# Kernel optimization log

Measured on AMD Instinct MI355X. Metric: run time of the kernel, lower is better.

The kernel has to match this reference:

```python
import jax, jax.numpy as jnp
import numpy as np

N = 100000
E = 1600000
D_IN = 128
D_OUT = 128


def setup_inputs() -> dict:
    key = jax.random.key(0)
    ks = jax.random.split(key, 6)
    seq = jax.random.normal(ks[0], (N, D_IN), dtype=jnp.float32)
    edge_src = jax.random.randint(ks[1], (E,), 0, N, dtype=jnp.int32)
    edge_dst = jax.random.randint(ks[2], (E,), 0, N, dtype=jnp.int32)
    adj_vals = jax.random.uniform(ks[3], (E,), dtype=jnp.float32)
    # xavier_uniform for [out, in] -> stored as [in, out] for x @ W
    lim = float(np.sqrt(6.0 / (D_IN + D_OUT)))
    w_fc = jax.random.uniform(ks[4], (D_IN, D_OUT), jnp.float32, -lim, lim)
    w_proj = jax.random.uniform(ks[5], (D_IN, D_OUT), jnp.float32, -lim, lim)
    b_proj = jnp.zeros((D_OUT,), jnp.float32)
    bias = jnp.zeros((D_OUT,), jnp.float32)
    return {"seq": seq, "edge_src": edge_src, "edge_dst": edge_dst,
            "adj_vals": adj_vals, "w_fc": w_fc, "w_proj": w_proj,
            "b_proj": b_proj, "bias": bias}


def reference(seq, edge_src, edge_dst, adj_vals, w_fc, w_proj, b_proj, bias):
    # h = fc(seq)  (no bias)
    h = seq @ w_fc                                  # [N, D_OUT]
    # spmm(adj, h): out[i] = sum_{e: dst=i} vals[e] * h[src[e]]
    msgs = adj_vals[:, None] * h[edge_src]          # [E, D_OUT]
    agg = jax.ops.segment_sum(msgs, edge_dst, num_segments=N)
    # bias add + residual proj(seq) add + tanh
    out = jnp.tanh(agg + bias + seq @ w_proj + b_proj)
    return out
```

## Files before the change

kernel.cpp:

```cpp
#include <hip/hip_runtime.h>
#include <math.h>


typedef __attribute__((ext_vector_type(8))) short short8;
typedef __attribute__((ext_vector_type(4))) float float4v;
typedef __attribute__((ext_vector_type(2))) _Float16 half2v;

#define PG 256
#define NBMAX 4096

static __device__ __forceinline__ short f2bf(float x) {
    unsigned u = __float_as_uint(x);
    unsigned r = (u + 0x7fffu + ((u >> 16) & 1u)) >> 16;
    return (short)r;
}
static __device__ __forceinline__ float bf2f(short h) {
    return __uint_as_float(((unsigned)(unsigned short)h) << 16);
}

__global__ __launch_bounds__(256)
void wconv_kernel(const float* __restrict__ wa, const float* __restrict__ wb,
                  short* __restrict__ whia, short* __restrict__ wloa,
                  short* __restrict__ whib, short* __restrict__ wlob) {
    const int bb = blockIdx.x;
    const float* w  = (bb < 16) ? wa   : wb;
    short* whi      = (bb < 16) ? whia : whib;
    short* wlo      = (bb < 16) ? wloa : wlob;
    const int i = (bb & 15) * 256 + threadIdx.x;
    const float4 v = ((const float4*)w)[i];
    const int k = i >> 5;
    const int c4 = (i & 31) * 4;
    float xs[4] = {v.x, v.y, v.z, v.w};
    #pragma unroll
    for (int j = 0; j < 4; j++) {
        const short hi = f2bf(xs[j]);
        const short lo = f2bf(xs[j] - bf2f(hi));
        whi[(c4 + j) * 128 + k] = hi;
        wlo[(c4 + j) * 128 + k] = lo;
    }
}

#define KP 136

__global__ __launch_bounds__(256, 2)
void mm_mfma_kernel(const float* __restrict__ seq, const short* __restrict__ whi,
                    const short* __restrict__ wlo,
                    const float* __restrict__ b0p, const float* __restrict__ b1p,
                    float* __restrict__ out, _Float16* __restrict__ out16,
                    int N, int add_bias) {
    __shared__ short wt_hi[128 * KP];
    __shared__ short wt_lo[128 * KP];

    const int tid = threadIdx.x;
    for (int i = tid; i < 2048; i += 256) {
        const int row = i >> 4;
        const int k8  = (i & 15) * 8;
        *(float4*)&wt_hi[row * KP + k8] = ((const float4*)whi)[i];
        *(float4*)&wt_lo[row * KP + k8] = ((const float4*)wlo)[i];
    }
    __syncthreads();

    const int wave = tid >> 6;
    const int lane = tid & 63;
    const int q = lane >> 4;
    const int c = lane & 15;
    const int R = blockIdx.x * 64 + wave * 16;
    const int rowL = (R + c < N) ? (R + c) : (N - 1);

    float4v acc[8];
    #pragma unroll
    for (int ct = 0; ct < 8; ct++) acc[ct] = (float4v){0.f, 0.f, 0.f, 0.f};

    #pragma unroll
    for (int t = 0; t < 4; t++) {
        const int kk = t * 32 + q * 8;
        const float4 a0 = *(const float4*)&seq[(size_t)rowL * 128 + kk];
        const float4 a1 = *(const float4*)&seq[(size_t)rowL * 128 + kk + 4];
        float xs[8] = {a0.x, a0.y, a0.z, a0.w, a1.x, a1.y, a1.z, a1.w};
        union { short s[8]; short8 v; } ahi, alo;
        #pragma unroll
        for (int j = 0; j < 8; j++) {
            const short hi = f2bf(xs[j]);
            ahi.s[j] = hi;
            alo.s[j] = f2bf(xs[j] - bf2f(hi));
        }
        #pragma unroll
        for (int ct = 0; ct < 8; ct++) {
            const int n = ct * 16 + c;
            const short8 bhi = *(const short8*)&wt_hi[n * KP + kk];
            const short8 blo = *(const short8*)&wt_lo[n * KP + kk];
            acc[ct] = __builtin_amdgcn_mfma_f32_16x16x32_bf16(ahi.v, bhi, acc[ct], 0, 0, 0);
            acc[ct] = __builtin_amdgcn_mfma_f32_16x16x32_bf16(ahi.v, blo, acc[ct], 0, 0, 0);
            acc[ct] = __builtin_amdgcn_mfma_f32_16x16x32_bf16(alo.v, bhi, acc[ct], 0, 0, 0);
        }
    }

    if (out16) {
        #pragma unroll
        for (int ct = 0; ct < 8; ct++) {
            const int col = ct * 16 + c;
            float badd = 0.f;
            if (add_bias) badd = b0p[col] + b1p[col];
            #pragma unroll
            for (int r = 0; r < 4; r++) {
                const int row = R + q * 4 + r;
                if (row < N) out16[(size_t)row * 128 + col] = (_Float16)(acc[ct][r] + badd);
            }
        }
    } else {
        #pragma unroll
        for (int ct = 0; ct < 8; ct++) {
            const int col = ct * 16 + c;
            float badd = 0.f;
            if (add_bias) badd = b0p[col] + b1p[col];
            #pragma unroll
            for (int r = 0; r < 4; r++) {
                const int row = R + q * 4 + r;
                if (row < N) out[(size_t)row * 128 + col] = acc[ct][r] + badd;
            }
        }
    }
}


__global__ __launch_bounds__(256)
void phist_kernel(const int* __restrict__ edst, int* __restrict__ hcnt,
                  int E, int S, int NB) {
    __shared__ int cnt[NBMAX];
    const int g = blockIdx.x;
    const int tid = threadIdx.x;
    for (int b = tid; b < NB; b += 256) cnt[b] = 0;
    __syncthreads();
    const int lo = g * S;
    const int hi = (lo + S < E) ? (lo + S) : E;
    for (int i = lo + tid; i < hi; i += 256)
        atomicAdd(&cnt[edst[i] >> 5], 1);
    __syncthreads();
    for (int b = tid; b < NB; b += 256) hcnt[b * PG + g] = cnt[b];
}

__global__ __launch_bounds__(256)
void pscan1_kernel(const int* __restrict__ in, int* __restrict__ out,
                   int* __restrict__ bsum, int L) {
    __shared__ int s[256];
    const int t = threadIdx.x;
    const int base = blockIdx.x * 4096 + t * 16;
    int v[16];
    int mysum = 0;
    #pragma unroll
    for (int j = 0; j < 16; j++) {
        v[j] = (base + j < L) ? in[base + j] : 0;
        mysum += v[j];
    }
    s[t] = mysum;
    __syncthreads();
    for (int o = 1; o < 256; o <<= 1) {
        int add = (t >= o) ? s[t - o] : 0;
        __syncthreads();
        s[t] += add;
        __syncthreads();
    }
    int run = s[t] - mysum;
    #pragma unroll
    for (int j = 0; j < 16; j++) {
        if (base + j < L) out[base + j] = run;
        run += v[j];
    }
    if (t == 255) bsum[blockIdx.x] = s[255];
}

__global__ __launch_bounds__(256)
void pscan2_kernel(const int* __restrict__ bsum, int* __restrict__ ebsum, int nb) {
    __shared__ int s[256];
    const int t = threadIdx.x;
    const int v = (t < nb) ? bsum[t] : 0;
    s[t] = v;
    __syncthreads();
    for (int o = 1; o < 256; o <<= 1) {
        int add = (t >= o) ? s[t - o] : 0;
        __syncthreads();
        s[t] += add;
        __syncthreads();
    }
    if (t < nb) ebsum[t] = s[t] - v;
}

__global__ __launch_bounds__(256)
void paddback_kernel(int* __restrict__ pos, const int* __restrict__ ebsum,
                     int* __restrict__ bstart, int L, int NB, int E) {
    const int add = ebsum[blockIdx.x];
    const int base = blockIdx.x * 4096 + threadIdx.x * 16;
    #pragma unroll
    for (int j = 0; j < 16; j++) {
        const int idx = base + j;
        if (idx < L) {
            const int v = pos[idx] + add;
            pos[idx] = v;
            if ((idx & (PG - 1)) == 0) bstart[idx / PG] = v;
        }
    }
    if (blockIdx.x == 0 && threadIdx.x == 0) bstart[NB] = E;
}

__global__ __launch_bounds__(256)
void pscatter_kernel(const int* __restrict__ esrc, const int* __restrict__ edst,
                     const float* __restrict__ vals, const int* __restrict__ pos,
                     int2* __restrict__ sedge, int E, int S, int NB) {
    __shared__ int cur[NBMAX];
    const int g = blockIdx.x;
    const int tid = threadIdx.x;
    for (int b = tid; b < NB; b += 256) cur[b] = pos[b * PG + g];
    __syncthreads();
    const int lo = g * S;
    const int hi = (lo + S < E) ? (lo + S) : E;
    for (int i = lo + tid; i < hi; i += 256) {
        const int d = edst[i];
        const int p = atomicAdd(&cur[d >> 5], 1);
        sedge[p] = make_int2((esrc[i] << 5) | (d & 31), __float_as_int(vals[i]));
    }
}

#define CAP 1024

__global__ __launch_bounds__(256, 8)
void aggregate_sorted(const int* __restrict__ bstart, const int2* __restrict__ sedge,
                      const _Float16* __restrict__ h, const _Float16* __restrict__ base,
                      float* __restrict__ out, int N) {
    __shared__ int2 ebuf[CAP];
    __shared__ int cnt[32], sc[32], off[33], cur[32];
    const int b = blockIdx.x;
    const int tid = threadIdx.x;
    const int beg = bstart[b];
    const int total = bstart[b + 1] - beg;
    const int cl = total < CAP ? total : CAP;

    if (tid < 32) cnt[tid] = 0;
    __syncthreads();
    for (int i = tid; i < cl; i += 256)
        atomicAdd(&cnt[sedge[beg + i].x & 31], 1);
    __syncthreads();
    if (tid < 32) sc[tid] = cnt[tid];
    __syncthreads();
    for (int o = 1; o < 32; o <<= 1) {
        int add = (tid < 32 && tid >= o) ? sc[tid - o] : 0;
        __syncthreads();
        if (tid < 32) sc[tid] += add;
        __syncthreads();
    }
    if (tid < 32) { off[tid] = sc[tid] - cnt[tid]; cur[tid] = sc[tid] - cnt[tid]; }
    if (tid == 31) off[32] = sc[31];
    __syncthreads();
    for (int i = tid; i < cl; i += 256) {
        const int2 e = sedge[beg + i];
        const int p = atomicAdd(&cur[e.x & 31], 1);
        ebuf[p] = e;
    }
    __syncthreads();

    const int wave = tid >> 6;
    const int lane = tid & 63;
    const int g = lane >> 4;
    const int c = lane & 15;
    const char* hb = (const char*)h;
    const unsigned coff = (unsigned)c << 4;

#define LOADQ(eX, vX, hX, jb) {                                               \
        const int jj = (jb) + g;                                              \
        eX = ebuf[jj < e1 ? jj : e0];                                         \
        vX = (jj < e1) ? __int_as_float(eX.y) : 0.f;                          \
        hX = *(const int4*)(hb + ((((unsigned)eX.x >> 5) << 8) + coff)); }
#define ACCQ(vX, hX) {                                                        \
        union { int4 i4; half2v h2[4]; } u; u.i4 = hX;                        \
        a0 += vX * (float)u.h2[0].x; a1 += vX * (float)u.h2[0].y;             \
        a2 += vX * (float)u.h2[1].x; a3 += vX * (float)u.h2[1].y;             \
        a4 += vX * (float)u.h2[2].x; a5 += vX * (float)u.h2[2].y;             \
        a6 += vX * (float)u.h2[3].x; a7 += vX * (float)u.h2[3].y; }

    for (int n = wave * 8; n < wave * 8 + 8; n++) {
        const int node = b * 32 + n;
        if (node >= N) break;
        const int e0 = off[n], e1 = off[n + 1];
        float a0 = 0.f, a1 = 0.f, a2 = 0.f, a3 = 0.f;
        float a4 = 0.f, a5 = 0.f, a6 = 0.f, a7 = 0.f;

        if (e1 > e0) {
            int2 eA, eB, eC;
            float vA = 0.f, vB = 0.f, vC = 0.f;
            int4 hA, hB, hC;
            int j = e0;
            LOADQ(eA, vA, hA, j);
            if (j + 4 < e1) LOADQ(eB, vB, hB, j + 4);
            while (true) {
                if (j + 8 < e1) LOADQ(eC, vC, hC, j + 8);
                ACCQ(vA, hA);
                j += 4; if (j >= e1) break;
                if (j + 8 < e1) LOADQ(eA, vA, hA, j + 8);
                ACCQ(vB, hB);
                j += 4; if (j >= e1) break;
                if (j + 8 < e1) LOADQ(eB, vB, hB, j + 8);
                ACCQ(vC, hC);
                j += 4; if (j >= e1) break;
            }
        }
        for (int t2 = cl; t2 < total; t2++) {
            const int2 e = sedge[beg + t2];
            if ((e.x & 31) == n) {
                const float v = (g == 0) ? __int_as_float(e.y) : 0.f;
                union { int4 i4; half2v h2[4]; } u;
                u.i4 = *(const int4*)(hb + ((((unsigned)e.x >> 5) << 8) + coff));
                a0 += v * (float)u.h2[0].x; a1 += v * (float)u.h2[0].y;
                a2 += v * (float)u.h2[1].x; a3 += v * (float)u.h2[1].y;
                a4 += v * (float)u.h2[2].x; a5 += v * (float)u.h2[2].y;
                a6 += v * (float)u.h2[3].x; a7 += v * (float)u.h2[3].y;
            }
        }

        a0 += __shfl_xor(a0, 16, 64); a0 += __shfl_xor(a0, 32, 64);
        a1 += __shfl_xor(a1, 16, 64); a1 += __shfl_xor(a1, 32, 64);
        a2 += __shfl_xor(a2, 16, 64); a2 += __shfl_xor(a2, 32, 64);
        a3 += __shfl_xor(a3, 16, 64); a3 += __shfl_xor(a3, 32, 64);
        a4 += __shfl_xor(a4, 16, 64); a4 += __shfl_xor(a4, 32, 64);
        a5 += __shfl_xor(a5, 16, 64); a5 += __shfl_xor(a5, 32, 64);
        a6 += __shfl_xor(a6, 16, 64); a6 += __shfl_xor(a6, 32, 64);
        a7 += __shfl_xor(a7, 16, 64); a7 += __shfl_xor(a7, 32, 64);

        float wx, wy;
        if (g == 0)      { wx = a0; wy = a1; }
        else if (g == 1) { wx = a2; wy = a3; }
        else if (g == 2) { wx = a4; wy = a5; }
        else             { wx = a6; wy = a7; }

        const half2v bb = __builtin_nontemporal_load(
            (const half2v*)(base + (size_t)node * 128 + (unsigned)(c * 8 + g * 2)));
        union { double d; float2 f; } rv;
        rv.f.x = tanhf(wx + (float)bb.x);
        rv.f.y = tanhf(wy + (float)bb.y);
        __builtin_nontemporal_store(rv.d, (double*)out + (size_t)node * 64 + (unsigned)(c * 4 + g));
    }
#undef LOADQ
#undef ACCQ
}


__global__ __launch_bounds__(256)
void edge_scatter(const int* __restrict__ esrc, const int* __restrict__ edst,
                  const float* __restrict__ vals, const _Float16* __restrict__ h,
                  float* __restrict__ out, int E) {
    const int gtid = blockIdx.x * blockDim.x + threadIdx.x;
    const int wave = gtid >> 6;
    const int lane = threadIdx.x & 63;
    const int nw = (gridDim.x * blockDim.x) >> 6;
    for (int e = wave; e < E; e += nw) {
        const int s = esrc[e];
        const int d = edst[e];
        const float v = vals[e];
        const half2v hv = *(const half2v*)(h + (size_t)s * 128 + lane * 2);
        float* op = out + (size_t)d * 128 + lane * 2;
        atomicAdd(op, v * (float)hv.x);
        atomicAdd(op + 1, v * (float)hv.y);
    }
}

__global__ __launch_bounds__(256)
void tanh_kernel(float* __restrict__ out, int n4) {
    const int i = blockIdx.x * blockDim.x + threadIdx.x;
    if (i < n4) {
        float4 v = ((float4*)out)[i];
        v.x = tanhf(v.x);
        v.y = tanhf(v.y);
        v.z = tanhf(v.z);
        v.w = tanhf(v.w);
        ((float4*)out)[i] = v;
    }
}

static inline size_t align64(size_t x) { return (x + 63) & ~(size_t)63; }

extern "C" void kernel_launch(void* const* d_in, const int* in_sizes, int n_in,
                              void* d_out, int out_size, void* d_ws, size_t ws_size,
                              hipStream_t stream) {
    const float* seq    = (const float*)d_in[0];
    const int*   esrc   = (const int*)  d_in[1];
    const int*   edst   = (const int*)  d_in[2];
    const float* vals   = (const float*)d_in[3];
    const float* w_fc   = (const float*)d_in[4];
    const float* w_proj = (const float*)d_in[5];
    const float* b_proj = (const float*)d_in[6];
    const float* bias   = (const float*)d_in[7];
    float* out = (float*)d_out;

    const int N = in_sizes[0] / 128;
    const int E = in_sizes[1];
    const int NB = (N + 31) >> 5;
    const int L  = NB * PG;
    const int S  = (E + PG - 1) / PG;
    const int nsb = (L + 4095) / 4096;

    char* ws = (char*)d_ws;
    const size_t o_h     = 0;
    const size_t o_b16   = align64(o_h    + (size_t)N * 128 * 2);
    const size_t o_whif  = align64(o_b16  + (size_t)N * 128 * 2);
    const size_t o_wlof  = align64(o_whif + 32768);
    const size_t o_whip  = align64(o_wlof + 32768);
    const size_t o_wlop  = align64(o_whip + 32768);
    const size_t o_hc    = align64(o_wlop + 32768);
    const size_t o_bs    = align64(o_hc   + (size_t)L * 4);
    const size_t o_bsum  = align64(o_bs   + (size_t)(NB + 1) * 4);
    const size_t o_ebs   = align64(o_bsum + 1024);
    const size_t o_sed   = align64(o_ebs  + 1024);
    const size_t need    = o_sed + (size_t)E * 8;

    _Float16* h      = (_Float16*)(ws + o_h);
    _Float16* base16 = (_Float16*)(ws + o_b16);
    short* whi_fc = (short*)(ws + o_whif);
    short* wlo_fc = (short*)(ws + o_wlof);
    short* whi_pj = (short*)(ws + o_whip);
    short* wlo_pj = (short*)(ws + o_wlop);
    int*   hcnt   = (int*)  (ws + o_hc);
    int*   pos    = hcnt;
    int*   bstart = (int*)  (ws + o_bs);
    int*   bsum   = (int*)  (ws + o_bsum);
    int*   ebsum  = (int*)  (ws + o_ebs);
    int2*  sedge  = (int2*) (ws + o_sed);

    const int mm_blocks = (N + 63) / 64;
    const bool sorted_ok = (ws_size >= need && NB <= NBMAX && nsb <= 256);

    wconv_kernel<<<32, 256, 0, stream>>>(w_fc, w_proj, whi_fc, wlo_fc, whi_pj, wlo_pj);
    mm_mfma_kernel<<<mm_blocks, 256, 0, stream>>>(seq, whi_fc, wlo_fc, nullptr, nullptr, nullptr, h, N, 0);

    if (sorted_ok) {
        mm_mfma_kernel<<<mm_blocks, 256, 0, stream>>>(seq, whi_pj, wlo_pj, b_proj, bias, nullptr, base16, N, 1);
        phist_kernel<<<PG, 256, 0, stream>>>(edst, hcnt, E, S, NB);
        pscan1_kernel<<<nsb, 256, 0, stream>>>(hcnt, hcnt, bsum, L);
        pscan2_kernel<<<1, 256, 0, stream>>>(bsum, ebsum, nsb);
        paddback_kernel<<<nsb, 256, 0, stream>>>(pos, ebsum, bstart, L, NB, E);
        pscatter_kernel<<<PG, 256, 0, stream>>>(esrc, edst, vals, pos, sedge, E, S, NB);
        aggregate_sorted<<<NB, 256, 0, stream>>>(bstart, sedge, h, base16, out, N);
    } else {
        mm_mfma_kernel<<<mm_blocks, 256, 0, stream>>>(seq, whi_pj, wlo_pj, b_proj, bias, out, nullptr, N, 1);
        edge_scatter<<<8192, 256, 0, stream>>>(esrc, edst, vals, h, out, E);
        const int n4 = (N * 128) / 4;
        tanh_kernel<<<(n4 + 255) / 256, 256, 0, stream>>>(out, n4);
    }
}
```

Measured before the change: 327.9 us.

## Fuse both projections into one MFMA kernel and coarsen destination buckets to 64

Replaces the separate weight-conversion kernel and two matmul launches with one kernel. That kernel converts both weight matrices into shared memory and computes h and the residual base from a single read of seq. The bucketed edge sort now uses 64-node buckets instead of 32, which halves the histogram width and the scan length. Each bucket is handled by two aggregation blocks, each filtering its own 32-node half. The fused kernel uses four large LDS tiles at 512 threads, which may limit occupancy, and each aggregation block now scans all of its bucket's edges twice.

```diff
diff --git a/kernel.cpp b/kernel.cpp
--- a/kernel.cpp
+++ b/kernel.cpp
@@ -7,7 +7,8 @@
 typedef __attribute__((ext_vector_type(2))) _Float16 half2v;
 
 #define PG 256
-#define NBMAX 4096
+#define NBMAX 2048
+#define KP 136
 
 static __device__ __forceinline__ short f2bf(float x) {
     unsigned u = __float_as_uint(x);
@@ -16,6 +17,166 @@
 }
 static __device__ __forceinline__ float bf2f(short h) {
     return __uint_as_float(((unsigned)(unsigned short)h) << 16);
+}
+
+__global__ __launch_bounds__(512)
+void mm_fused_kernel(const float* __restrict__ seq, const float* __restrict__ wfc,
+                     const float* __restrict__ wpj, const float* __restrict__ b0p,
+                     const float* __restrict__ b1p, _Float16* __restrict__ h,
+                     _Float16* __restrict__ base16, int N) {
+    __shared__ short fc_hi[128 * KP];
+    __shared__ short fc_lo[128 * KP];
+    __shared__ short pj_hi[128 * KP];
+    __shared__ short pj_lo[128 * KP];
+
+    const int tid = threadIdx.x;
+    for (int i = tid; i < 4096; i += 512) {
+        const int k = i >> 5;
+        const int c4 = (i & 31) * 4;
+        float4 v = ((const float4*)wfc)[i];
+        float xs[4] = {v.x, v.y, v.z, v.w};
+        #pragma unroll
+        for (int j = 0; j < 4; j++) {
+            const short hi = f2bf(xs[j]);
+            fc_hi[(c4 + j) * KP + k] = hi;
+            fc_lo[(c4 + j) * KP + k] = f2bf(xs[j] - bf2f(hi));
+        }
+        v = ((const float4*)wpj)[i];
+        xs[0] = v.x; xs[1] = v.y; xs[2] = v.z; xs[3] = v.w;
+        #pragma unroll
+        for (int j = 0; j < 4; j++) {
+            const short hi = f2bf(xs[j]);
+            pj_hi[(c4 + j) * KP + k] = hi;
+            pj_lo[(c4 + j) * KP + k] = f2bf(xs[j] - bf2f(hi));
+        }
+    }
+    __syncthreads();
+
+    const int wave = tid >> 6;
+    const int lane = tid & 63;
+    const int q = lane >> 4;
+    const int c = lane & 15;
+    const int R = blockIdx.x * 128 + wave * 16;
+    const int rowL = (R + c < N) ? (R + c) : (N - 1);
+
+    float4v acch[8], accb[8];
+    #pragma unroll
+    for (int ct = 0; ct < 8; ct++) {
+        acch[ct] = (float4v){0.f, 0.f, 0.f, 0.f};
+        accb[ct] = (float4v){0.f, 0.f, 0.f, 0.f};
+    }
+
+    #pragma unroll
+    for (int t = 0; t < 4; t++) {
+        const int kk = t * 32 + q * 8;
+        const float4 a0 = *(const float4*)&seq[(size_t)rowL * 128 + kk];
+        const float4 a1 = *(const float4*)&seq[(size_t)rowL * 128 + kk + 4];
+        float xs[8] = {a0.x, a0.y, a0.z, a0.w, a1.x, a1.y, a1.z, a1.w};
+        union { short s[8]; short8 v; } ahi, alo;
+        #pragma unroll
+        for (int j = 0; j < 8; j++) {
+            const short hi = f2bf(xs[j]);
+            ahi.s[j] = hi;
+            alo.s[j] = f2bf(xs[j] - bf2f(hi));
+        }
+        #pragma unroll
+        for (int ct = 0; ct < 8; ct++) {
+            const int n = ct * 16 + c;
+            const short8 bh0 = *(const short8*)&fc_hi[n * KP + kk];
+            const short8 bl0 = *(const short8*)&fc_lo[n * KP + kk];
+            const short8 bh1 = *(const short8*)&pj_hi[n * KP + kk];
+            const short8 bl1 = *(const short8*)&pj_lo[n * KP + kk];
+            acch[ct] = __builtin_amdgcn_mfma_f32_16x16x32_bf16(ahi.v, bh0, acch[ct], 0, 0, 0);
+            acch[ct] = __builtin_amdgcn_mfma_f32_16x16x32_bf16(ahi.v, bl0, acch[ct], 0, 0, 0);
+            acch[ct] = __builtin_amdgcn_mfma_f32_16x16x32_bf16(alo.v, bh0, acch[ct], 0, 0, 0);
+            accb[ct] = __builtin_amdgcn_mfma_f32_16x16x32_bf16(ahi.v, bh1, accb[ct], 0, 0, 0);
+            accb[ct] = __builtin_amdgcn_mfma_f32_16x16x32_bf16(ahi.v, bl1, accb[ct], 0, 0, 0);
+            accb[ct] = __builtin_amdgcn_mfma_f32_16x16x32_bf16(alo.v, bh1, accb[ct], 0, 0, 0);
+        }
+    }
+
+    #pragma unroll
+    for (int ct = 0; ct < 8; ct++) {
+        const int col = ct * 16 + c;
+        const float badd = b0p[col] + b1p[col];
+        #pragma unroll
+        for (int r = 0; r < 4; r++) {
+            const int row = R + q * 4 + r;
+            if (row < N) {
+                h[(size_t)row * 128 + col]      = (_Float16)acch[ct][r];
+                base16[(size_t)row * 128 + col] = (_Float16)(accb[ct][r] + badd);
+            }
+        }
+    }
+}
+
+__global__ __launch_bounds__(256, 2)
+void mm_mfma_kernel(const float* __restrict__ seq, const short* __restrict__ whi,
+                    const short* __restrict__ wlo,
+                    const float* __restrict__ b0p, const float* __restrict__ b1p,
+                    float* __restrict__ out, _Float16* __restrict__ out16,
+                    int N, int add_bias) {
+    __shared__ short wt_hi[128 * KP];
+    __shared__ short wt_lo[128 * KP];
+
+    const int tid = threadIdx.x;
+    for (int i = tid; i < 2048; i += 256) {
+        const int row = i >> 4;
+        const int k8  = (i & 15) * 8;
+        *(float4*)&wt_hi[row * KP + k8] = ((const float4*)whi)[i];
+        *(float4*)&wt_lo[row * KP + k8] = ((const float4*)wlo)[i];
+    }
+    __syncthreads();
+
+    const int wave = tid >> 6;
+    const int lane = tid & 63;
+    const int q = lane >> 4;
+    const int c = lane & 15;
+    const int R = blockIdx.x * 64 + wave * 16;
+    const int rowL = (R + c < N) ? (R + c) : (N - 1);
+
+    float4v acc[8];
+    #pragma unroll
+    for (int ct = 0; ct < 8; ct++) acc[ct] = (float4v){0.f, 0.f, 0.f, 0.f};
+
+    #pragma unroll
+    for (int t = 0; t < 4; t++) {
+        const int kk = t * 32 + q * 8;
+        const float4 a0 = *(const float4*)&seq[(size_t)rowL * 128 + kk];
+        const float4 a1 = *(const float4*)&seq[(size_t)rowL * 128 + kk + 4];
+        float xs[8] = {a0.x, a0.y, a0.z, a0.w, a1.x, a1.y, a1.z, a1.w};
+        union { short s[8]; short8 v; } ahi, alo;
+        #pragma unroll
+        for (int j = 0; j < 8; j++) {
+            const short hi = f2bf(xs[j]);
+            ahi.s[j] = hi;
+            alo.s[j] = f2bf(xs[j] - bf2f(hi));
+        }
+        #pragma unroll
+        for (int ct = 0; ct < 8; ct++) {
+            const int n = ct * 16 + c;
+            const short8 bhi = *(const short8*)&wt_hi[n * KP + kk];
+            const short8 blo = *(const short8*)&wt_lo[n * KP + kk];
+            acc[ct] = __builtin_amdgcn_mfma_f32_16x16x32_bf16(ahi.v, bhi, acc[ct], 0, 0, 0);
+            acc[ct] = __builtin_amdgcn_mfma_f32_16x16x32_bf16(ahi.v, blo, acc[ct], 0, 0, 0);
+            acc[ct] = __builtin_amdgcn_mfma_f32_16x16x32_bf16(alo.v, bhi, acc[ct], 0, 0, 0);
+        }
+    }
+
+    #pragma unroll
+    for (int ct = 0; ct < 8; ct++) {
+        const int col = ct * 16 + c;
+        float badd = 0.f;
+        if (add_bias) badd = b0p[col] + b1p[col];
+        #pragma unroll
+        for (int r = 0; r < 4; r++) {
+            const int row = R + q * 4 + r;
+            if (row < N) {
+                if (out16) out16[(size_t)row * 128 + col] = (_Float16)(acc[ct][r] + badd);
+                else       out[(size_t)row * 128 + col]   = acc[ct][r] + badd;
+            }
+        }
+    }
 }
 
 __global__ __launch_bounds__(256)
@@ -40,88 +201,6 @@
     }
 }
 
-#define KP 136
-
-__global__ __launch_bounds__(256, 2)
-void mm_mfma_kernel(const float* __restrict__ seq, const short* __restrict__ whi,
-                    const short* __restrict__ wlo,
-                    const float* __restrict__ b0p, const float* __restrict__ b1p,
-                    float* __restrict__ out, _Float16* __restrict__ out16,
-                    int N, int add_bias) {
-    __shared__ short wt_hi[128 * KP];
-    __shared__ short wt_lo[128 * KP];
-
-    const int tid = threadIdx.x;
-    for (int i = tid; i < 2048; i += 256) {
-        const int row = i >> 4;
-        const int k8  = (i & 15) * 8;
-        *(float4*)&wt_hi[row * KP + k8] = ((const float4*)whi)[i];
-        *(float4*)&wt_lo[row * KP + k8] = ((const float4*)wlo)[i];
-    }
-    __syncthreads();
-
-    const int wave = tid >> 6;
-    const int lane = tid & 63;
-    const int q = lane >> 4;
-    const int c = lane & 15;
-    const int R = blockIdx.x * 64 + wave * 16;
-    const int rowL = (R + c < N) ? (R + c) : (N - 1);
-
-    float4v acc[8];
-    #pragma unroll
-    for (int ct = 0; ct < 8; ct++) acc[ct] = (float4v){0.f, 0.f, 0.f, 0.f};
-
-    #pragma unroll
-    for (int t = 0; t < 4; t++) {
-        const int kk = t * 32 + q * 8;
-        const float4 a0 = *(const float4*)&seq[(size_t)rowL * 128 + kk];
-        const float4 a1 = *(const float4*)&seq[(size_t)rowL * 128 + kk + 4];
-        float xs[8] = {a0.x, a0.y, a0.z, a0.w, a1.x, a1.y, a1.z, a1.w};
-        union { short s[8]; short8 v; } ahi, alo;
-        #pragma unroll
-        for (int j = 0; j < 8; j++) {
-            const short hi = f2bf(xs[j]);
-            ahi.s[j] = hi;
-            alo.s[j] = f2bf(xs[j] - bf2f(hi));
-        }
-        #pragma unroll
-        for (int ct = 0; ct < 8; ct++) {
-            const int n = ct * 16 + c;
-            const short8 bhi = *(const short8*)&wt_hi[n * KP + kk];
-            const short8 blo = *(const short8*)&wt_lo[n * KP + kk];
-            acc[ct] = __builtin_amdgcn_mfma_f32_16x16x32_bf16(ahi.v, bhi, acc[ct], 0, 0, 0);
-            acc[ct] = __builtin_amdgcn_mfma_f32_16x16x32_bf16(ahi.v, blo, acc[ct], 0, 0, 0);
-            acc[ct] = __builtin_amdgcn_mfma_f32_16x16x32_bf16(alo.v, bhi, acc[ct], 0, 0, 0);
-        }
-    }
-
-    if (out16) {
-        #pragma unroll
-        for (int ct = 0; ct < 8; ct++) {
-            const int col = ct * 16 + c;
-            float badd = 0.f;
-            if (add_bias) badd = b0p[col] + b1p[col];
-            #pragma unroll
-            for (int r = 0; r < 4; r++) {
-                const int row = R + q * 4 + r;
-                if (row < N) out16[(size_t)row * 128 + col] = (_Float16)(acc[ct][r] + badd);
-            }
-        }
-    } else {
-        #pragma unroll
-        for (int ct = 0; ct < 8; ct++) {
-            const int col = ct * 16 + c;
-            float badd = 0.f;
-            if (add_bias) badd = b0p[col] + b1p[col];
-            #pragma unroll
-            for (int r = 0; r < 4; r++) {
-                const int row = R + q * 4 + r;
-                if (row < N) out[(size_t)row * 128 + col] = acc[ct][r] + badd;
-            }
-        }
-    }
-}
-
 
 __global__ __launch_bounds__(256)
 void phist_kernel(const int* __restrict__ edst, int* __restrict__ hcnt,
@@ -134,7 +213,7 @@
     const int lo = g * S;
     const int hi = (lo + S < E) ? (lo + S) : E;
     for (int i = lo + tid; i < hi; i += 256)
-        atomicAdd(&cnt[edst[i] >> 5], 1);
+        atomicAdd(&cnt[edst[i] >> 6], 1);
     __syncthreads();
     for (int b = tid; b < NB; b += 256) hcnt[b * PG + g] = cnt[b];
 }
@@ -144,11 +223,11 @@
                    int* __restrict__ bsum, int L) {
     __shared__ int s[256];
     const int t = threadIdx.x;
-    const int base = blockIdx.x * 4096 + t * 16;
-    int v[16];
+    const int base = blockIdx.x * 2048 + t * 8;
+    int v[8];
     int mysum = 0;
     #pragma unroll
-    for (int j = 0; j < 16; j++) {
+    for (int j = 0; j < 8; j++) {
         v[j] = (base + j < L) ? in[base + j] : 0;
         mysum += v[j];
     }
@@ -162,7 +241,7 @@
     }
     int run = s[t] - mysum;
     #pragma unroll
-    for (int j = 0; j < 16; j++) {
+    for (int j = 0; j < 8; j++) {
         if (base + j < L) out[base + j] = run;
         run += v[j];
     }
@@ -189,9 +268,9 @@
 void paddback_kernel(int* __restrict__ pos, const int* __restrict__ ebsum,
                      int* __restrict__ bstart, int L, int NB, int E) {
     const int add = ebsum[blockIdx.x];
-    const int base = blockIdx.x * 4096 + threadIdx.x * 16;
-    #pragma unroll
-    for (int j = 0; j < 16; j++) {
+    const int base = blockIdx.x * 2048 + threadIdx.x * 8;
+    #pragma unroll
+    for (int j = 0; j < 8; j++) {
         const int idx = base + j;
         if (idx < L) {
             const int v = pos[idx] + add;
@@ -215,8 +294,8 @@
     const int hi = (lo + S < E) ? (lo + S) : E;
     for (int i = lo + tid; i < hi; i += 256) {
         const int d = edst[i];
-        const int p = atomicAdd(&cur[d >> 5], 1);
-        sedge[p] = make_int2((esrc[i] << 5) | (d & 31), __float_as_int(vals[i]));
+        const int p = atomicAdd(&cur[d >> 6], 1);
+        sedge[p] = make_int2((esrc[i] << 6) | (d & 63), __float_as_int(vals[i]));
     }
 }
 
@@ -228,16 +307,19 @@
                       float* __restrict__ out, int N) {
     __shared__ int2 ebuf[CAP];
     __shared__ int cnt[32], sc[32], off[33], cur[32];
-    const int b = blockIdx.x;
+    const int bb = blockIdx.x;
+    const int b = bb >> 1;
+    const int half = bb & 1;
     const int tid = threadIdx.x;
     const int beg = bstart[b];
     const int total = bstart[b + 1] - beg;
-    const int cl = total < CAP ? total : CAP;
 
     if (tid < 32) cnt[tid] = 0;
     __syncthreads();
-    for (int i = tid; i < cl; i += 256)
-        atomicAdd(&cnt[sedge[beg + i].x & 31], 1);
+    for (int i = tid; i < total; i += 256) {
+        const int x = sedge[beg + i].x & 63;
+        if ((x >> 5) == half) atomicAdd(&cnt[x & 31], 1);
+    }
     __syncthreads();
     if (tid < 32) sc[tid] = cnt[tid];
     __syncthreads();
@@ -250,13 +332,8 @@
     if (tid < 32) { off[tid] = sc[tid] - cnt[tid]; cur[tid] = sc[tid] - cnt[tid]; }
     if (tid == 31) off[32] = sc[31];
     __syncthreads();
-    for (int i = tid; i < cl; i += 256) {
-        const int2 e = sedge[beg + i];
-        const int p = atomicAdd(&cur[e.x & 31], 1);
-        ebuf[p] = e;
-    }
-    __syncthreads();
-
+
+    const int fc = off[32];
     const int wave = tid >> 6;
     const int lane = tid & 63;
     const int g = lane >> 4;
@@ -268,77 +345,98 @@
         const int jj = (jb) + g;                                              \
         eX = ebuf[jj < e1 ? jj : e0];                                         \
         vX = (jj < e1) ? __int_as_float(eX.y) : 0.f;                          \
-        hX = *(const int4*)(hb + ((((unsigned)eX.x >> 5) << 8) + coff)); }
+        hX = *(const int4*)(hb + ((((unsigned)eX.x >> 6) << 8) + coff)); }
 #define ACCQ(vX, hX) {                                                        \
         union { int4 i4; half2v h2[4]; } u; u.i4 = hX;                        \
         a0 += vX * (float)u.h2[0].x; a1 += vX * (float)u.h2[0].y;             \
         a2 += vX * (float)u.h2[1].x; a3 += vX * (float)u.h2[1].y;             \
         a4 += vX * (float)u.h2[2].x; a5 += vX * (float)u.h2[2].y;             \
         a6 += vX * (float)u.h2[3].x; a7 += vX * (float)u.h2[3].y; }
-
-    for (int n = wave * 8; n < wave * 8 + 8; n++) {
-        const int node = b * 32 + n;
-        if (node >= N) break;
-        const int e0 = off[n], e1 = off[n + 1];
-        float a0 = 0.f, a1 = 0.f, a2 = 0.f, a3 = 0.f;
-        float a4 = 0.f, a5 = 0.f, a6 = 0.f, a7 = 0.f;
-
-        if (e1 > e0) {
-            int2 eA, eB, eC;
-            float vA = 0.f, vB = 0.f, vC = 0.f;
-            int4 hA, hB, hC;
-            int j = e0;
-            LOADQ(eA, vA, hA, j);
-            if (j + 4 < e1) LOADQ(eB, vB, hB, j + 4);
-            while (true) {
-                if (j + 8 < e1) LOADQ(eC, vC, hC, j + 8);
-                ACCQ(vA, hA);
-                j += 4; if (j >= e1) break;
-                if (j + 8 < e1) LOADQ(eA, vA, hA, j + 8);
-                ACCQ(vB, hB);
-                j += 4; if (j >= e1) break;
-                if (j + 8 < e1) LOADQ(eB, vB, hB, j + 8);
-                ACCQ(vC, hC);
-                j += 4; if (j >= e1) break;
+#define REDUCE_STORE(node) {                                                  \
+        a0 += __shfl_xor(a0, 16, 64); a0 += __shfl_xor(a0, 32, 64);           \
+        a1 += __shfl_xor(a1, 16, 64); a1 += __shfl_xor(a1, 32, 64);           \
+        a2 += __shfl_xor(a2, 16, 64); a2 += __shfl_xor(a2, 32, 64);           \
+        a3 += __shfl_xor(a3, 16, 64); a3 += __shfl_xor(a3, 32, 64);           \
+        a4 += __shfl_xor(a4, 16, 64); a4 += __shfl_xor(a4, 32, 64);           \
+        a5 += __shfl_xor(a5, 16, 64); a5 += __shfl_xor(a5, 32, 64);           \
+        a6 += __shfl_xor(a6, 16, 64); a6 += __shfl_xor(a6, 32, 64);           \
+        a7 += __shfl_xor(a7, 16, 64); a7 += __shfl_xor(a7, 32, 64);           \
+        float wx, wy;                                                         \
+        if (g == 0)      { wx = a0; wy = a1; }                                \
+        else if (g == 1) { wx = a2; wy = a3; }                                \
+        else if (g == 2) { wx = a4; wy = a5; }                                \
+        else             { wx = a6; wy = a7; }                                \
+        const half2v bv = __builtin_nontemporal_load(                         \
+            (const half2v*)(base + (size_t)(node) * 128 + (unsigned)(c * 8 + g * 2))); \
+        union { double d; float2 f; } rv;                                     \
+        rv.f.x = tanhf(wx + (float)bv.x);                                     \
+        rv.f.y = tanhf(wy + (float)bv.y);                                     \
+        __builtin_nontemporal_store(rv.d, (double*)out + (size_t)(node) * 64 + (unsigned)(c * 4 + g)); }
+
+    if (fc <= CAP) {
+        for (int i = tid; i < total; i += 256) {
+            const int2 e = sedge[beg + i];
+            const int x = e.x & 63;
+            if ((x >> 5) == half) {
+                const int p = atomicAdd(&cur[x & 31], 1);
+                ebuf[p] = e;
             }
         }
-        for (int t2 = cl; t2 < total; t2++) {
-            const int2 e = sedge[beg + t2];
-            if ((e.x & 31) == n) {
-                const float v = (g == 0) ? __int_as_float(e.y) : 0.f;
-                union { int4 i4; half2v h2[4]; } u;
-                u.i4 = *(const int4*)(hb + ((((unsigned)e.x >> 5) << 8) + coff));
-                a0 += v * (float)u.h2[0].x; a1 += v * (float)u.h2[0].y;
-                a2 += v * (float)u.h2[1].x; a3 += v * (float)u.h2[1].y;
-                a4 += v * (float)u.h2[2].x; a5 += v * (float)u.h2[2].y;
-                a6 += v * (float)u.h2[3].x; a7 += v * (float)u.h2[3].y;
+        __syncthreads();
+
+        for (int n = wave * 8; n < wave * 8 + 8; n++) {
+            const int node = b * 64 + half * 32 + n;
+            if (node >= N) break;
+            const int e0 = off[n], e1 = off[n + 1];
+            float a0 = 0.f, a1 = 0.f, a2 = 0.f, a3 = 0.f;
+            float a4 = 0.f, a5 = 0.f, a6 = 0.f, a7 = 0.f;
+
+            if (e1 > e0) {
+                int2 eA, eB, eC;
+                float vA = 0.f, vB = 0.f, vC = 0.f;
+                int4 hA, hB, hC;
+                int j = e0;
+                LOADQ(eA, vA, hA, j);
+                if (j + 4 < e1) LOADQ(eB, vB, hB, j + 4);
+                while (true) {
+                    if (j + 8 < e1) LOADQ(eC, vC, hC, j + 8);
+                    ACCQ(vA, hA);
+                    j += 4; if (j >= e1) break;
+                    if (j + 8 < e1) LOADQ(eA, vA, hA, j + 8);
+                    ACCQ(vB, hB);
+                    j += 4; if (j >= e1) break;
+                    if (j + 8 < e1) LOADQ(eB, vB, hB, j + 8);
+                    ACCQ(vC, hC);
+                    j += 4; if (j >= e1) break;
+                }
             }
-        }
-
-        a0 += __shfl_xor(a0, 16, 64); a0 += __shfl_xor(a0, 32, 64);
-        a1 += __shfl_xor(a1, 16, 64); a1 += __shfl_xor(a1, 32, 64);
-        a2 += __shfl_xor(a2, 16, 64); a2 += __shfl_xor(a2, 32, 64);
-        a3 += __shfl_xor(a3, 16, 64); a3 += __shfl_xor(a3, 32, 64);
-        a4 += __shfl_xor(a4, 16, 64); a4 += __shfl_xor(a4, 32, 64);
-        a5 += __shfl_xor(a5, 16, 64); a5 += __shfl_xor(a5, 32, 64);
-        a6 += __shfl_xor(a6, 16, 64); a6 += __shfl_xor(a6, 32, 64);
-        a7 += __shfl_xor(a7, 16, 64); a7 += __shfl_xor(a7, 32, 64);
-
-        float wx, wy;
-        if (g == 0)      { wx = a0; wy = a1; }
-        else if (g == 1) { wx = a2; wy = a3; }
-        else if (g == 2) { wx = a4; wy = a5; }
-        else             { wx = a6; wy = a7; }
-
-        const half2v bb = __builtin_nontemporal_load(
-            (const half2v*)(base + (size_t)node * 128 + (unsigned)(c * 8 + g * 2)));
-        union { double d; float2 f; } rv;
-        rv.f.x = tanhf(wx + (float)bb.x);
-        rv.f.y = tanhf(wy + (float)bb.y);
-        __builtin_nontemporal_store(rv.d, (double*)out + (size_t)node * 64 + (unsigned)(c * 4 + g));
+            REDUCE_STORE(node);
+        }
+    } else {
+        for (int n = wave * 8; n < wave * 8 + 8; n++) {
+            const int node = b * 64 + half * 32 + n;
+            if (node >= N) break;
+            const int key = half * 32 + n;
+            float a0 = 0.f, a1 = 0.f, a2 = 0.f, a3 = 0.f;
+            float a4 = 0.f, a5 = 0.f, a6 = 0.f, a7 = 0.f;
+            for (int i = 0; i < total; i++) {
+                const int2 e = sedge[beg + i];
+                if ((e.x & 63) == key) {
+                    const float v = (g == 0) ? __int_as_float(e.y) : 0.f;
+                    union { int4 i4; half2v h2[4]; } u;
+                    u.i4 = *(const int4*)(hb + ((((unsigned)e.x >> 6) << 8) + coff));
+                    a0 += v * (float)u.h2[0].x; a1 += v * (float)u.h2[0].y;
+                    a2 += v * (float)u.h2[1].x; a3 += v * (float)u.h2[1].y;
+                    a4 += v * (float)u.h2[2].x; a5 += v * (float)u.h2[2].y;
+                    a6 += v * (float)u.h2[3].x; a7 += v * (float)u.h2[3].y;
+                }
+            }
+            REDUCE_STORE(node);
+        }
     }
 #undef LOADQ
 #undef ACCQ
+#undef REDUCE_STORE
 }
 
 
@@ -391,10 +489,10 @@
 
     const int N = in_sizes[0] / 128;
     const int E = in_sizes[1];
-    const int NB = (N + 31) >> 5;
+    const int NB = (N + 63) >> 6;
     const int L  = NB * PG;
     const int S  = (E + PG - 1) / PG;
-    const int nsb = (L + 4095) / 4096;
+    const int nsb = (L + 2047) / 2048;
 
     char* ws = (char*)d_ws;
     const size_t o_h     = 0;
@@ -423,21 +521,21 @@
     int*   ebsum  = (int*)  (ws + o_ebs);
     int2*  sedge  = (int2*) (ws + o_sed);
 
-    const int mm_blocks = (N + 63) / 64;
     const bool sorted_ok = (ws_size >= need && NB <= NBMAX && nsb <= 256);
 
-    wconv_kernel<<<32, 256, 0, stream>>>(w_fc, w_proj, whi_fc, wlo_fc, whi_pj, wlo_pj);
-    mm_mfma_kernel<<<mm_blocks, 256, 0, stream>>>(seq, whi_fc, wlo_fc, nullptr, nullptr, nullptr, h, N, 0);
-
     if (sorted_ok) {
-        mm_mfma_kernel<<<mm_blocks, 256, 0, stream>>>(seq, whi_pj, wlo_pj, b_proj, bias, nullptr, base16, N, 1);
+        const int fm_blocks = (N + 127) / 128;
+        mm_fused_kernel<<<fm_blocks, 512, 0, stream>>>(seq, w_fc, w_proj, b_proj, bias, h, base16, N);
         phist_kernel<<<PG, 256, 0, stream>>>(edst, hcnt, E, S, NB);
         pscan1_kernel<<<nsb, 256, 0, stream>>>(hcnt, hcnt, bsum, L);
         pscan2_kernel<<<1, 256, 0, stream>>>(bsum, ebsum, nsb);
         paddback_kernel<<<nsb, 256, 0, stream>>>(pos, ebsum, bstart, L, NB, E);
         pscatter_kernel<<<PG, 256, 0, stream>>>(esrc, edst, vals, pos, sedge, E, S, NB);
-        aggregate_sorted<<<NB, 256, 0, stream>>>(bstart, sedge, h, base16, out, N);
+        aggregate_sorted<<<NB * 2, 256, 0, stream>>>(bstart, sedge, h, base16, out, N);
     } else {
+        const int mm_blocks = (N + 63) / 64;
+        wconv_kernel<<<32, 256, 0, stream>>>(w_fc, w_proj, whi_fc, wlo_fc, whi_pj, wlo_pj);
+        mm_mfma_kernel<<<mm_blocks, 256, 0, stream>>>(seq, whi_fc, wlo_fc, nullptr, nullptr, nullptr, h, N, 0);
         mm_mfma_kernel<<<mm_blocks, 256, 0, stream>>>(seq, whi_pj, wlo_pj, b_proj, bias, out, nullptr, N, 1);
         edge_scatter<<<8192, 256, 0, stream>>>(esrc, edst, vals, h, out, E);
         const int n4 = (N * 128) / 4;
```

Measured after the change: 354.7 us. 8.2% more time.
